# Kernel tuning notes

Measured on AMD Instinct MI355X. Metric: run time of the kernel, lower is better.

## Reference

```python
import jax, jax.numpy as jnp
import numpy as np

B, T, C, H = 2, 2048, 1024, 16
D = C // H  # head dim, even
NEG = -1e10  # masked_fill value used by the torch module (not -inf)


def _rope_cache(dim, max_positions):
    # Faithful to source: theta_i = 1/10000**(-2*(i-1)/dim), i = arange(dim//2)
    i = jnp.arange(dim // 2, dtype=jnp.float32)
    theta = 1.0 / (10000.0 ** (-2.0 * (i - 1.0) / dim))
    ang = jnp.arange(max_positions, dtype=jnp.float32)[:, None] * theta[None, :]  # [T, D/2]
    return jnp.cos(ang), jnp.sin(ang)


def _apply_rope(x, cos, sin):
    # x: [B,H,T,D]; consecutive pairs form complex numbers (x[...,2j], x[...,2j+1])
    xp = x.reshape(*x.shape[:-1], D // 2, 2)
    xr, xi = xp[..., 0], xp[..., 1]
    rr = xr * cos - xi * sin
    ri = xr * sin + xi * cos
    return jnp.stack([rr, ri], axis=-1).reshape(x.shape)


def setup_inputs() -> dict:
    key = jax.random.key(0)
    ks = jax.random.split(key, 5)
    s = 1.0 / np.sqrt(C)
    return {
        'x': jax.random.normal(ks[0], (B, T, C), jnp.float32),
        'Wq': jax.random.normal(ks[1], (C, C), jnp.float32) * s,
        'bq': jnp.zeros((C,), jnp.float32),
        'Wk': jax.random.normal(ks[2], (C, C), jnp.float32) * s,
        'bk': jnp.zeros((C,), jnp.float32),
        'Wv': jax.random.normal(ks[3], (C, C), jnp.float32) * s,
        'bv': jnp.zeros((C,), jnp.float32),
        'Wp': jax.random.normal(ks[4], (C, C), jnp.float32) * s,
        'bp': jnp.zeros((C,), jnp.float32),
    }


def reference(x, Wq, bq, Wk, bk, Wv, bv, Wp, bp):
    cos, sin = _rope_cache(D, T)  # [T, D/2]
    def split_heads(h):
        return h.reshape(B, T, H, D).transpose(0, 2, 1, 3)  # [B,H,T,D]
    q = split_heads(x @ Wq.T + bq)
    k = split_heads(x @ Wk.T + bk)
    v = split_heads(x @ Wv.T + bv)
    q = _apply_rope(q, cos, sin)
    k = _apply_rope(k, cos, sin)
    att = jnp.einsum('bhqd,bhkd->bhqk', q, k) * (1.0 / np.sqrt(D))  # [B,H,T,T]
    causal = jnp.tril(jnp.ones((T, T), bool))
    att = jnp.where(causal, att, NEG)
    att = jax.nn.softmax(att, axis=-1)
    y = jnp.einsum('bhqk,bhkd->bhqd', att, v)
    y = y.transpose(0, 2, 1, 3).reshape(B, T, C)
    return y @ Wp.T + bp
```

## Files before the change

kernel.cpp:

```cpp
#include <hip/hip_runtime.h>

#define SEQ 2048
#define CDIM 1024
#define NHEAD 16
#define HDIM 64

typedef __bf16 bf16x8 __attribute__((ext_vector_type(8)));
typedef __bf16 bf16x4v __attribute__((ext_vector_type(4)));
typedef float f32x4 __attribute__((ext_vector_type(4)));

typedef const __attribute__((address_space(1))) char* gcp_t;
typedef __attribute__((address_space(3))) char* lcp_t;

__device__ __forceinline__ void gload16(const void* g, void* l) {
    __builtin_amdgcn_global_load_lds((gcp_t)g, (lcp_t)l, 16, 0, 0);
}

__device__ __forceinline__ unsigned short f2bf(float f) {
    unsigned int u = __float_as_uint(f);
    u += 0x7fffu + ((u >> 16) & 1u);
    return (unsigned short)(u >> 16);
}


__global__ void cvt_kernel(const float* __restrict__ src, unsigned short* __restrict__ dst, int n4) {
    int i = blockIdx.x * blockDim.x + threadIdx.x;
    if (i < n4) {
        float4 v = ((const float4*)src)[i];
        ushort4 o;
        o.x = f2bf(v.x); o.y = f2bf(v.y); o.z = f2bf(v.z); o.w = f2bf(v.w);
        ((ushort4*)dst)[i] = o;
    }
}

__global__ void cvtw_kernel(const float* __restrict__ Wq, const float* __restrict__ Wk,
                            const float* __restrict__ Wv, const float* __restrict__ Wp,
                            unsigned short* __restrict__ wqkv, unsigned short* __restrict__ wpb) {
    int i = blockIdx.x * blockDim.x + threadIdx.x;
    int which = i >> 18, r = i & 262143;
    const float* s = (which == 0) ? Wq : (which == 1) ? Wk : (which == 2) ? Wv : Wp;
    unsigned short* d = (which < 3) ? (wqkv + (size_t)which * 1048576) : wpb;
    float4 v = ((const float4*)s)[r];
    ushort4 o;
    o.x = f2bf(v.x); o.y = f2bf(v.y); o.z = f2bf(v.z); o.w = f2bf(v.w);
    ((ushort4*)d)[r] = o;
}

__global__ void rope_kernel(float2* __restrict__ cstab) {
    int idx = blockIdx.x * blockDim.x + threadIdx.x;
    int j = idx & 31, t = idx >> 5;
    float e = -2.0f * ((float)j - 1.0f) / 64.0f;
    float denom = (float)pow(10000.0, (double)e);
    float theta = 1.0f / denom;
    float ang = (float)t * theta;
    cstab[idx] = make_float2(cosf(ang), sinf(ang));
}

template <int MODE>
__global__ __launch_bounds__(256) void gemm_bt(
    const unsigned short* __restrict__ A, const unsigned short* __restrict__ Bm,
    const float* __restrict__ b0, const float* __restrict__ b1, const float* __restrict__ b2,
    unsigned short* __restrict__ qb, unsigned short* __restrict__ kb,
    unsigned short* __restrict__ vtb, float* __restrict__ outf,
    const float2* __restrict__ cstab)
{
    constexpr int K = 1024;
    constexpr int NIT = K / 32;
    __shared__ __align__(16) unsigned short As[2][128 * 32];
    __shared__ __align__(16) unsigned short Bs[2][128 * 32];
    const int tid = threadIdx.x, lane = tid & 63, wid = tid >> 6;
    const int m0 = blockIdx.y * 128, n0 = blockIdx.x * 128;
    const int wr = wid >> 1, wc = wid & 1;

    f32x4 acc[4][4] = {};

    const char* Ag = (const char*)(A + (size_t)m0 * K);
    const char* Bg = (const char*)(Bm + (size_t)n0 * K);
    const int r0 = tid >> 2, cb = (tid & 3) * 16;
    const int r1 = r0 + 64;
    const int ldsw = wid << 10;

    auto stage = [&](int k0, int bufi) {
        gload16(Ag + (size_t)r0 * 2048 + k0 * 2 + cb, (char*)As[bufi] + ldsw);
        gload16(Ag + (size_t)r1 * 2048 + k0 * 2 + cb, (char*)As[bufi] + 4096 + ldsw);
        gload16(Bg + (size_t)r0 * 2048 + k0 * 2 + cb, (char*)Bs[bufi] + ldsw);
        gload16(Bg + (size_t)r1 * 2048 + k0 * 2 + cb, (char*)Bs[bufi] + 4096 + ldsw);
    };

    stage(0, 0);
    __syncthreads();

    for (int it = 0; it < NIT; ++it) {
        const int cur = it & 1;
        if (it + 1 < NIT) stage((it + 1) * 32, cur ^ 1);
        bf16x8 af[4], bfr[4];
#pragma unroll
        for (int am = 0; am < 4; ++am)
            af[am] = *(const bf16x8*)(As[cur] + (wr * 64 + am * 16 + (lane & 15)) * 32 + (lane >> 4) * 8);
#pragma unroll
        for (int an = 0; an < 4; ++an)
            bfr[an] = *(const bf16x8*)(Bs[cur] + (wc * 64 + an * 16 + (lane & 15)) * 32 + (lane >> 4) * 8);
#pragma unroll
        for (int am = 0; am < 4; ++am)
#pragma unroll
            for (int an = 0; an < 4; ++an)
                acc[am][an] = __builtin_amdgcn_mfma_f32_16x16x32_bf16(af[am], bfr[an], acc[am][an], 0, 0, 0);
        __syncthreads();
    }

    if (MODE == 0) {
        const float QSCL = 0.18033688011112042f;
#pragma unroll
        for (int an = 0; an < 4; ++an) {
            const int ng = n0 + wc * 64 + an * 16 + (lane & 15);
            const int which = ng >> 10, nl = ng & 1023;
            const int h = nl >> 6, d = nl & 63;
            const float* bptr = (which == 0) ? b0 : (which == 1) ? b1 : b2;
            const float bias = bptr[nl];
            if (which < 2) {
                unsigned short* dst = (which == 0) ? qb : kb;
                const float qs = (which == 0) ? QSCL : 1.0f;
                const int j = d >> 1;
#pragma unroll
                for (int am = 0; am < 4; ++am) {
#pragma unroll
                    for (int i = 0; i < 4; ++i) {
                        const int row = m0 + wr * 64 + am * 16 + (lane >> 4) * 4 + i;
                        const int bb = row >> 11, t = row & 2047;
                        float v = acc[am][an][i] + bias;
                        float p = __shfl_xor(v, 1);
                        const float2 cs = cstab[t * 32 + j];
                        v = (d & 1) ? fmaf(v, cs.x, p * cs.y) : fmaf(v, cs.x, -p * cs.y);
                        dst[((size_t)((bb * 16 + h) * 2048 + t)) * 64 + d] = f2bf(v * qs);
                    }
                }
            } else {
#pragma unroll
                for (int am = 0; am < 4; ++am) {
                    const int rowb = m0 + wr * 64 + am * 16 + (lane >> 4) * 4;
                    const int bb = rowb >> 11, t = rowb & 2047;
                    ushort4 pk;
                    pk.x = f2bf(acc[am][an][0] + bias);
                    pk.y = f2bf(acc[am][an][1] + bias);
                    pk.z = f2bf(acc[am][an][2] + bias);
                    pk.w = f2bf(acc[am][an][3] + bias);
                    *(ushort4*)(vtb + ((size_t)((bb * 16 + h) * 64 + d)) * 2048 + t) = pk;
                }
            }
        }
    } else {
#pragma unroll
        for (int an = 0; an < 4; ++an) {
            const int col = n0 + wc * 64 + an * 16 + (lane & 15);
            const float bias = b0[col];
#pragma unroll
            for (int am = 0; am < 4; ++am)
#pragma unroll
                for (int i = 0; i < 4; ++i) {
                    const int row = m0 + wr * 64 + am * 16 + (lane >> 4) * 4 + i;
                    outf[(size_t)row * 1024 + col] = acc[am][an][i] + bias;
                }
        }
    }
}

__global__ __launch_bounds__(256) void attn_kernel(
    const unsigned short* __restrict__ qb, const unsigned short* __restrict__ kb,
    const unsigned short* __restrict__ vtb, unsigned short* __restrict__ yb)
{
    __shared__ __align__(16) unsigned short Ks[2][64 * 64];
    __shared__ __align__(16) unsigned short Vs[2][64 * 64];
    __shared__ __align__(16) unsigned short Ps[4][16 * 64];
    const int tid = threadIdx.x, lane = tid & 63, wid = tid >> 6;
    const int bh = blockIdx.y;
    const int b = bh >> 4, h = bh & 15;
    const int qt = (bh & 16) ? (31 - blockIdx.x) : blockIdx.x;
    const int q0 = qt * 64;
    const int qw = q0 + wid * 16;
    const unsigned short* Qg = qb + (size_t)bh * SEQ * HDIM;
    const char* Kg = (const char*)(kb + (size_t)bh * SEQ * HDIM);
    const char* Vg = (const char*)(vtb + (size_t)bh * HDIM * SEQ);

    bf16x8 qf[2];
#pragma unroll
    for (int kf = 0; kf < 2; ++kf)
        qf[kf] = *(const bf16x8*)(Qg + (size_t)(qw + (lane & 15)) * 64 + kf * 32 + (lane >> 4) * 8);

    f32x4 o[4] = {};
    float mrun = -3e38f;
    float lrun = 0.0f;

    const int nt = qt + 1;
    const int cr0 = tid >> 3, cc0 = ((tid & 7) * 16) ^ ((cr0 & 7) << 4);
    const int cr1 = cr0 + 32, cc1 = ((tid & 7) * 16) ^ ((cr1 & 7) << 4);
    const int ldsw = wid << 10;

    auto stage = [&](int kt, int bufi) {
        const size_t kv0 = (size_t)kt * 64;
        gload16(Kg + (kv0 + cr0) * 128 + cc0, (char*)Ks[bufi] + ldsw);
        gload16(Kg + (kv0 + cr1) * 128 + cc1, (char*)Ks[bufi] + 4096 + ldsw);
        gload16(Vg + (size_t)cr0 * 4096 + kv0 * 2 + cc0, (char*)Vs[bufi] + ldsw);
        gload16(Vg + (size_t)cr1 * 4096 + kv0 * 2 + cc1, (char*)Vs[bufi] + 4096 + ldsw);
    };

    stage(0, 0);
    __syncthreads();

    for (int kt = 0; kt < nt; ++kt) {
        const int cur = kt & 1;
        if (kt + 1 < nt) stage(kt + 1, cur ^ 1);
        const int kv0 = kt * 64;
        {
            f32x4 s[4] = {};
            __builtin_amdgcn_s_setprio(1);
#pragma unroll
            for (int kf = 0; kf < 2; ++kf) {
                bf16x8 kfr[4];
#pragma unroll
                for (int an = 0; an < 4; ++an) {
                    const int r = an * 16 + (lane & 15);
                    kfr[an] = *(const bf16x8*)((const char*)Ks[cur] + r * 128 + ((kf * 64 + (lane >> 4) * 16) ^ ((r & 7) << 4)));
                }
#pragma unroll
                for (int an = 0; an < 4; ++an)
                    s[an] = __builtin_amdgcn_mfma_f32_16x16x32_bf16(kfr[an], qf[kf], s[an], 0, 0, 0);
            }
            __builtin_amdgcn_s_setprio(0);
            const bool need_mask = (kv0 + 63 > qw);
            const int qg = qw + (lane & 15);
            const int kbase = kv0 + ((lane >> 4) << 2);
            float p[4][4];
            float mx = -3e38f;
#pragma unroll
            for (int an = 0; an < 4; ++an)
#pragma unroll
                for (int i = 0; i < 4; ++i) {
                    float v = s[an][i];
                    if (need_mask && (kbase + an * 16 + i > qg)) v = -3e38f;
                    p[an][i] = v;
                    mx = fmaxf(mx, v);
                }
            mx = fmaxf(mx, __shfl_xor(mx, 16));
            mx = fmaxf(mx, __shfl_xor(mx, 32));
            if (!__all(mx <= mrun + 8.0f)) {
                const float mnew = fmaxf(mrun, mx);
                const float fsc = __builtin_amdgcn_exp2f(mrun - mnew);
                lrun *= fsc;
#pragma unroll
                for (int dn = 0; dn < 4; ++dn) o[dn] *= fsc;
                mrun = mnew;
            }
            float rs = 0.0f;
#pragma unroll
            for (int an = 0; an < 4; ++an)
#pragma unroll
                for (int i = 0; i < 4; ++i) {
                    p[an][i] = __builtin_amdgcn_exp2f(p[an][i] - mrun);
                    rs += p[an][i];
                }
            rs += __shfl_xor(rs, 16);
            rs += __shfl_xor(rs, 32);
            lrun += rs;
            const int ql = lane & 15;
            char* pb = (char*)Ps[wid] + ql * 128;
            const int xr = (ql & 7) << 4;
            const int gb = (lane >> 4) << 3;
#pragma unroll
            for (int an = 0; an < 4; ++an) {
                bf16x4v pk;
                pk[0] = (__bf16)p[an][0]; pk[1] = (__bf16)p[an][1];
                pk[2] = (__bf16)p[an][2]; pk[3] = (__bf16)p[an][3];
                *(bf16x4v*)(pb + ((an * 32 + gb) ^ xr)) = pk;
            }
            __builtin_amdgcn_s_setprio(1);
#pragma unroll
            for (int kf = 0; kf < 2; ++kf) {
                bf16x8 vf[4], pf;
#pragma unroll
                for (int dn = 0; dn < 4; ++dn) {
                    const int r = dn * 16 + (lane & 15);
                    vf[dn] = *(const bf16x8*)((const char*)Vs[cur] + r * 128 + ((kf * 64 + (lane >> 4) * 16) ^ ((r & 7) << 4)));
                }
                {
                    const int qlr = lane & 15;
                    pf = *(const bf16x8*)((const char*)Ps[wid] + qlr * 128 + ((kf * 64 + (lane >> 4) * 16) ^ ((qlr & 7) << 4)));
                }
#pragma unroll
                for (int dn = 0; dn < 4; ++dn)
                    o[dn] = __builtin_amdgcn_mfma_f32_16x16x32_bf16(vf[dn], pf, o[dn], 0, 0, 0);
            }
            __builtin_amdgcn_s_setprio(0);
        }
        __syncthreads();
    }

    {
        const float inv = 1.0f / lrun;
        const int qg = qw + (lane & 15);
        unsigned short* yrow = yb + (size_t)(b * SEQ + qg) * CDIM + h * 64;
#pragma unroll
        for (int dn = 0; dn < 4; ++dn) {
            const int d = dn * 16 + ((lane >> 4) << 2);
            bf16x4v pk;
            pk[0] = (__bf16)(o[dn][0] * inv);
            pk[1] = (__bf16)(o[dn][1] * inv);
            pk[2] = (__bf16)(o[dn][2] * inv);
            pk[3] = (__bf16)(o[dn][3] * inv);
            *(bf16x4v*)(yrow + d) = pk;
        }
    }
}


extern "C" void kernel_launch(void* const* d_in, const int* in_sizes, int n_in,
                              void* d_out, int out_size, void* d_ws, size_t ws_size,
                              hipStream_t stream) {
    (void)in_sizes; (void)n_in; (void)out_size; (void)ws_size;
    const float* x  = (const float*)d_in[0];
    const float* Wq = (const float*)d_in[1];
    const float* bq = (const float*)d_in[2];
    const float* Wk = (const float*)d_in[3];
    const float* bk = (const float*)d_in[4];
    const float* Wv = (const float*)d_in[5];
    const float* bv = (const float*)d_in[6];
    const float* Wp = (const float*)d_in[7];
    const float* bp = (const float*)d_in[8];
    float* out = (float*)d_out;

    char* ws = (char*)d_ws;
    size_t off = 0;
    auto take = [&](size_t bytes) -> char* {
        char* p = ws + off;
        off = (off + bytes + 255) & ~(size_t)255;
        return p;
    };
    float2* cstab = (float2*)take((size_t)SEQ * 32 * 8);
    unsigned short* xb   = (unsigned short*)take((size_t)4096 * 1024 * 2);
    unsigned short* wqkv = (unsigned short*)take((size_t)3 * 1024 * 1024 * 2);
    unsigned short* wpb  = (unsigned short*)take((size_t)1024 * 1024 * 2);
    unsigned short* qbuf = (unsigned short*)take((size_t)32 * SEQ * HDIM * 2);
    unsigned short* kbuf = (unsigned short*)take((size_t)32 * SEQ * HDIM * 2);
    unsigned short* vtb  = (unsigned short*)take((size_t)32 * HDIM * SEQ * 2);
    unsigned short* yb   = (unsigned short*)take((size_t)4096 * 1024 * 2);

    rope_kernel<<<256, 256, 0, stream>>>(cstab);
    cvt_kernel<<<4096, 256, 0, stream>>>(x, xb, 1048576);
    cvtw_kernel<<<4096, 256, 0, stream>>>(Wq, Wk, Wv, Wp, wqkv, wpb);

    dim3 g0(24, 32);
    gemm_bt<0><<<g0, 256, 0, stream>>>(xb, wqkv, bq, bk, bv, qbuf, kbuf, vtb, nullptr, cstab);
    dim3 g1(32, 32);
    attn_kernel<<<g1, 256, 0, stream>>>(qbuf, kbuf, vtb, yb);
    dim3 g2(8, 32);
    gemm_bt<1><<<g2, 256, 0, stream>>>(yb, wpb, bp, nullptr, nullptr, nullptr, nullptr, nullptr, out, cstab);
}
```

Before: 139.5 us.

## Fuse conversion kernels, swizzle GEMM LDS, use 64-row tiles for output projection

Merges the three preprocessing launches (RoPE table, x conversion, weight conversion) into one kernel to cut launch overhead. Adds an XOR swizzle to the GEMM shared-memory layout, applied through the global-to-LDS load addresses, to reduce bank conflicts on fragment reads. Templates the GEMM on the M tile so the output projection runs with 64-row tiles and twice as many blocks for better CU occupancy, at the cost of less B-tile reuse per block.

```diff
diff --git a/kernel.cpp b/kernel.cpp
--- a/kernel.cpp
+++ b/kernel.cpp
@@ -22,41 +22,42 @@
     return (unsigned short)(u >> 16);
 }
 
-
-__global__ void cvt_kernel(const float* __restrict__ src, unsigned short* __restrict__ dst, int n4) {
+__device__ __forceinline__ int swz16(int r) { return ((r >> 1) & 3) << 4; }
+
+__global__ void cvt_rope_all(const float* __restrict__ x,
+                             const float* __restrict__ Wq, const float* __restrict__ Wk,
+                             const float* __restrict__ Wv, const float* __restrict__ Wp,
+                             unsigned short* __restrict__ xb,
+                             unsigned short* __restrict__ wqkv, unsigned short* __restrict__ wpb,
+                             float2* __restrict__ cstab) {
     int i = blockIdx.x * blockDim.x + threadIdx.x;
-    if (i < n4) {
-        float4 v = ((const float4*)src)[i];
+    if (i < 2097152) {
+        const float* s;
+        unsigned short* d;
+        int r;
+        if (i < 1048576) { s = x; d = xb; r = i; }
+        else {
+            int j = i - 1048576;
+            int which = j >> 18; r = j & 262143;
+            s = (which == 0) ? Wq : (which == 1) ? Wk : (which == 2) ? Wv : Wp;
+            d = (which < 3) ? (wqkv + (size_t)which * 1048576) : wpb;
+        }
+        float4 v = ((const float4*)s)[r];
         ushort4 o;
         o.x = f2bf(v.x); o.y = f2bf(v.y); o.z = f2bf(v.z); o.w = f2bf(v.w);
-        ((ushort4*)dst)[i] = o;
-    }
-}
-
-__global__ void cvtw_kernel(const float* __restrict__ Wq, const float* __restrict__ Wk,
-                            const float* __restrict__ Wv, const float* __restrict__ Wp,
-                            unsigned short* __restrict__ wqkv, unsigned short* __restrict__ wpb) {
-    int i = blockIdx.x * blockDim.x + threadIdx.x;
-    int which = i >> 18, r = i & 262143;
-    const float* s = (which == 0) ? Wq : (which == 1) ? Wk : (which == 2) ? Wv : Wp;
-    unsigned short* d = (which < 3) ? (wqkv + (size_t)which * 1048576) : wpb;
-    float4 v = ((const float4*)s)[r];
-    ushort4 o;
-    o.x = f2bf(v.x); o.y = f2bf(v.y); o.z = f2bf(v.z); o.w = f2bf(v.w);
-    ((ushort4*)d)[r] = o;
-}
-
-__global__ void rope_kernel(float2* __restrict__ cstab) {
-    int idx = blockIdx.x * blockDim.x + threadIdx.x;
-    int j = idx & 31, t = idx >> 5;
-    float e = -2.0f * ((float)j - 1.0f) / 64.0f;
-    float denom = (float)pow(10000.0, (double)e);
-    float theta = 1.0f / denom;
-    float ang = (float)t * theta;
-    cstab[idx] = make_float2(cosf(ang), sinf(ang));
-}
-
-template <int MODE>
+        ((ushort4*)d)[r] = o;
+    } else {
+        int idx = i - 2097152;
+        int j = idx & 31, t = idx >> 5;
+        float e = -2.0f * ((float)j - 1.0f) / 64.0f;
+        float denom = (float)pow(10000.0, (double)e);
+        float theta = 1.0f / denom;
+        float ang = (float)t * theta;
+        cstab[idx] = make_float2(cosf(ang), sinf(ang));
+    }
+}
+
+template <int MODE, int BM>
 __global__ __launch_bounds__(256) void gemm_bt(
     const unsigned short* __restrict__ A, const unsigned short* __restrict__ Bm,
     const float* __restrict__ b0, const float* __restrict__ b1, const float* __restrict__ b2,
@@ -66,25 +67,29 @@
 {
     constexpr int K = 1024;
     constexpr int NIT = K / 32;
-    __shared__ __align__(16) unsigned short As[2][128 * 32];
-    __shared__ __align__(16) unsigned short Bs[2][128 * 32];
+    constexpr int NR = (BM == 128) ? 4 : 2;
+    __shared__ __align__(16) char As[2][BM * 64];
+    __shared__ __align__(16) char Bs[2][128 * 64];
     const int tid = threadIdx.x, lane = tid & 63, wid = tid >> 6;
-    const int m0 = blockIdx.y * 128, n0 = blockIdx.x * 128;
-    const int wr = wid >> 1, wc = wid & 1;
-
-    f32x4 acc[4][4] = {};
+    const int m0 = blockIdx.y * BM, n0 = blockIdx.x * 128;
+    const int wr = (BM == 128) ? ((wid >> 1) * 64) : 0;
+    const int wc = (BM == 128) ? ((wid & 1) * 64) : (wid * 32);
+
+    f32x4 acc[4][NR] = {};
 
     const char* Ag = (const char*)(A + (size_t)m0 * K);
     const char* Bg = (const char*)(Bm + (size_t)n0 * K);
     const int r0 = tid >> 2, cb = (tid & 3) * 16;
-    const int r1 = r0 + 64;
     const int ldsw = wid << 10;
 
     auto stage = [&](int k0, int bufi) {
-        gload16(Ag + (size_t)r0 * 2048 + k0 * 2 + cb, (char*)As[bufi] + ldsw);
-        gload16(Ag + (size_t)r1 * 2048 + k0 * 2 + cb, (char*)As[bufi] + 4096 + ldsw);
-        gload16(Bg + (size_t)r0 * 2048 + k0 * 2 + cb, (char*)Bs[bufi] + ldsw);
-        gload16(Bg + (size_t)r1 * 2048 + k0 * 2 + cb, (char*)Bs[bufi] + 4096 + ldsw);
+        char* Ad = As[bufi];
+        char* Bd = Bs[bufi];
+        gload16(Ag + (size_t)r0 * 2048 + k0 * 2 + (cb ^ swz16(r0)), Ad + ldsw);
+        if constexpr (BM == 128)
+            gload16(Ag + (size_t)(r0 + 64) * 2048 + k0 * 2 + (cb ^ swz16(r0 + 64)), Ad + 4096 + ldsw);
+        gload16(Bg + (size_t)r0 * 2048 + k0 * 2 + (cb ^ swz16(r0)), Bd + ldsw);
+        gload16(Bg + (size_t)(r0 + 64) * 2048 + k0 * 2 + (cb ^ swz16(r0 + 64)), Bd + 4096 + ldsw);
     };
 
     stage(0, 0);
@@ -93,17 +98,24 @@
     for (int it = 0; it < NIT; ++it) {
         const int cur = it & 1;
         if (it + 1 < NIT) stage((it + 1) * 32, cur ^ 1);
-        bf16x8 af[4], bfr[4];
+        const char* Ac = As[cur];
+        const char* Bc = Bs[cur];
+        const int fs = (lane >> 4) * 16;
+        bf16x8 af[4], bfr[NR];
+#pragma unroll
+        for (int am = 0; am < 4; ++am) {
+            const int r = wr + am * 16 + (lane & 15);
+            af[am] = *(const bf16x8*)(Ac + r * 64 + (fs ^ swz16(r)));
+        }
+#pragma unroll
+        for (int an = 0; an < NR; ++an) {
+            const int r = wc + an * 16 + (lane & 15);
+            bfr[an] = *(const bf16x8*)(Bc + r * 64 + (fs ^ swz16(r)));
+        }
 #pragma unroll
         for (int am = 0; am < 4; ++am)
-            af[am] = *(const bf16x8*)(As[cur] + (wr * 64 + am * 16 + (lane & 15)) * 32 + (lane >> 4) * 8);
-#pragma unroll
-        for (int an = 0; an < 4; ++an)
-            bfr[an] = *(const bf16x8*)(Bs[cur] + (wc * 64 + an * 16 + (lane & 15)) * 32 + (lane >> 4) * 8);
-#pragma unroll
-        for (int am = 0; am < 4; ++am)
-#pragma unroll
-            for (int an = 0; an < 4; ++an)
+#pragma unroll
+            for (int an = 0; an < NR; ++an)
                 acc[am][an] = __builtin_amdgcn_mfma_f32_16x16x32_bf16(af[am], bfr[an], acc[am][an], 0, 0, 0);
         __syncthreads();
     }
@@ -111,8 +123,8 @@
     if (MODE == 0) {
         const float QSCL = 0.18033688011112042f;
 #pragma unroll
-        for (int an = 0; an < 4; ++an) {
-            const int ng = n0 + wc * 64 + an * 16 + (lane & 15);
+        for (int an = 0; an < NR; ++an) {
+            const int ng = n0 + wc + an * 16 + (lane & 15);
             const int which = ng >> 10, nl = ng & 1023;
             const int h = nl >> 6, d = nl & 63;
             const float* bptr = (which == 0) ? b0 : (which == 1) ? b1 : b2;
@@ -125,7 +137,7 @@
                 for (int am = 0; am < 4; ++am) {
 #pragma unroll
                     for (int i = 0; i < 4; ++i) {
-                        const int row = m0 + wr * 64 + am * 16 + (lane >> 4) * 4 + i;
+                        const int row = m0 + wr + am * 16 + (lane >> 4) * 4 + i;
                         const int bb = row >> 11, t = row & 2047;
                         float v = acc[am][an][i] + bias;
                         float p = __shfl_xor(v, 1);
@@ -137,7 +149,7 @@
             } else {
 #pragma unroll
                 for (int am = 0; am < 4; ++am) {
-                    const int rowb = m0 + wr * 64 + am * 16 + (lane >> 4) * 4;
+                    const int rowb = m0 + wr + am * 16 + (lane >> 4) * 4;
                     const int bb = rowb >> 11, t = rowb & 2047;
                     ushort4 pk;
                     pk.x = f2bf(acc[am][an][0] + bias);
@@ -150,14 +162,14 @@
         }
     } else {
 #pragma unroll
-        for (int an = 0; an < 4; ++an) {
-            const int col = n0 + wc * 64 + an * 16 + (lane & 15);
+        for (int an = 0; an < NR; ++an) {
+            const int col = n0 + wc + an * 16 + (lane & 15);
             const float bias = b0[col];
 #pragma unroll
             for (int am = 0; am < 4; ++am)
 #pragma unroll
                 for (int i = 0; i < 4; ++i) {
-                    const int row = m0 + wr * 64 + am * 16 + (lane >> 4) * 4 + i;
+                    const int row = m0 + wr + am * 16 + (lane >> 4) * 4 + i;
                     outf[(size_t)row * 1024 + col] = acc[am][an][i] + bias;
                 }
         }
@@ -262,7 +274,7 @@
             rs += __shfl_xor(rs, 32);
             lrun += rs;
             const int ql = lane & 15;
-            char* pb = (char*)Ps[wid] + ql * 128;
+            char* pbs = (char*)Ps[wid] + ql * 128;
             const int xr = (ql & 7) << 4;
             const int gb = (lane >> 4) << 3;
 #pragma unroll
@@ -270,7 +282,7 @@
                 bf16x4v pk;
                 pk[0] = (__bf16)p[an][0]; pk[1] = (__bf16)p[an][1];
                 pk[2] = (__bf16)p[an][2]; pk[3] = (__bf16)p[an][3];
-                *(bf16x4v*)(pb + ((an * 32 + gb) ^ xr)) = pk;
+                *(bf16x4v*)(pbs + ((an * 32 + gb) ^ xr)) = pk;
             }
             __builtin_amdgcn_s_setprio(1);
 #pragma unroll
@@ -343,14 +355,12 @@
     unsigned short* vtb  = (unsigned short*)take((size_t)32 * HDIM * SEQ * 2);
     unsigned short* yb   = (unsigned short*)take((size_t)4096 * 1024 * 2);
 
-    rope_kernel<<<256, 256, 0, stream>>>(cstab);
-    cvt_kernel<<<4096, 256, 0, stream>>>(x, xb, 1048576);
-    cvtw_kernel<<<4096, 256, 0, stream>>>(Wq, Wk, Wv, Wp, wqkv, wpb);
+    cvt_rope_all<<<8448, 256, 0, stream>>>(x, Wq, Wk, Wv, Wp, xb, wqkv, wpb, cstab);
 
     dim3 g0(24, 32);
-    gemm_bt<0><<<g0, 256, 0, stream>>>(xb, wqkv, bq, bk, bv, qbuf, kbuf, vtb, nullptr, cstab);
+    gemm_bt<0, 128><<<g0, 256, 0, stream>>>(xb, wqkv, bq, bk, bv, qbuf, kbuf, vtb, nullptr, cstab);
     dim3 g1(32, 32);
     attn_kernel<<<g1, 256, 0, stream>>>(qbuf, kbuf, vtb, yb);
-    dim3 g2(8, 32);
-    gemm_bt<1><<<g2, 256, 0, stream>>>(yb, wpb, bp, nullptr, nullptr, nullptr, nullptr, nullptr, out, cstab);
-}
+    dim3 g2(8, 64);
+    gemm_bt<1, 64><<<g2, 256, 0, stream>>>(yb, wpb, bp, nullptr, nullptr, nullptr, nullptr, nullptr, out, cstab);
+}
```

Result: faster. 132.2 us (-5.2%).
